# Kernel tuning notes

Measured on AMD Instinct MI355X. Metric: run time of the kernel, lower is better.

The kernel has to match this reference:

```python
import jax, jax.numpy as jnp
import numpy as np
import math

N_HEAD = 16


def setup_inputs() -> dict:
    key = jax.random.key(0)
    ks = jax.random.split(key, 9)
    B, T, D = 2, 2048, 1024
    s = 1.0 / math.sqrt(D)
    return {
        "queries": jax.random.normal(ks[0], (B, T, D), jnp.float32),
        "keys": jax.random.normal(ks[1], (B, T, D), jnp.float32),
        "key_mask": jax.random.randint(ks[2], (B, T), 0, 2, jnp.int32),
        "Wq": jax.random.normal(ks[3], (D, D), jnp.float32) * s,
        "bq": jax.random.normal(ks[4], (D,), jnp.float32) * 0.01,
        "Wk": jax.random.normal(ks[5], (D, D), jnp.float32) * s,
        "bk": jax.random.normal(ks[6], (D,), jnp.float32) * 0.01,
        "Wv": jax.random.normal(ks[7], (D, D), jnp.float32) * s,
        "bv": jax.random.normal(ks[8], (D,), jnp.float32) * 0.01,
    }


def reference(queries, keys, key_mask, Wq, bq, Wk, bk, Wv, bv):
    B, Tq, D = queries.shape
    Tk = keys.shape[1]
    H = N_HEAD
    dk = D // H
    scale = 1.0 / math.sqrt(dk)

    # torch Linear: x @ W.T + b
    Q = (queries @ Wq.T + bq).reshape(B, Tq, H, dk)
    K = (keys @ Wk.T + bk).reshape(B, Tk, H, dk)
    V = (keys @ Wv.T + bv).reshape(B, Tk, H, dk)

    # flatten batch-major over (B, H) to match torch permute+reshape -> (B*H, T, dk)
    Qf = Q.transpose(0, 2, 1, 3).reshape(B * H, Tq, dk)
    Kf = K.transpose(0, 2, 1, 3).reshape(B * H, Tk, dk)
    Vf = V.transpose(0, 2, 1, 3).reshape(B * H, Tk, dk)

    scores = jnp.einsum("nqd,nkd->nqk", Qf, Kf) * scale  # (B*H, Tq, Tk)

    # torch builds masks via .repeat(n_head,1,1): HEAD-major tiling (H copies of B).
    # flat row i of scores has batch i//H but receives mask of batch i%B —
    # reproduced faithfully here.
    km = jnp.tile(key_mask, (H, 1))  # (H*B, Tk), row j -> key_mask[j % B]
    scores = jnp.where(km[:, None, :] == 0, -1e9, scores)

    attn = jax.nn.softmax(scores, axis=-1)
    qm = jnp.tile(key_mask, (H, 1))[:, :, None].astype(attn.dtype)  # (H*B, Tk, 1), Tq==Tk
    attn = attn * qm

    # dropout: identity in eval mode
    out = jnp.einsum("nqk,nkd->nqd", attn, Vf)  # (B*H, Tq, dk)
    out = out.reshape(B, H, Tq, dk).transpose(0, 2, 1, 3).reshape(B, Tq, D)
    return out
```

## Files before the change

### kernel.cpp

```cpp
#include <hip/hip_runtime.h>
#include <hip/hip_bf16.h>

typedef __attribute__((ext_vector_type(8))) short bf16x8;
typedef __attribute__((ext_vector_type(4))) short bf16x4;
typedef __attribute__((ext_vector_type(4))) float f32x4;
typedef __attribute__((ext_vector_type(16))) float f32x16;
typedef __attribute__((ext_vector_type(4))) unsigned u32x4;

__device__ inline short f2bf(float f) {
    unsigned u = __builtin_bit_cast(unsigned, f);
    u += 0x7FFF + ((u >> 16) & 1);
    return (short)(u >> 16);
}


__global__ __launch_bounds__(256) void cvt_bf16(
    const float* __restrict__ xq, const float* __restrict__ xk,
    const float* __restrict__ Wq, const float* __restrict__ Wk,
    const float* __restrict__ Wv, const int* __restrict__ key_mask,
    short* __restrict__ ws)
{
    const int blk = blockIdx.x;
    if (blk >= 11264) {
        float* bias = (float*)(ws + 24117248u);
        const int i0 = threadIdx.x * 4;
#pragma unroll
        for (int p = 0; p < 4; ++p) {
            int idx = p * 1024 + i0;
            int4 m = *(const int4*)&key_mask[idx];
            f32x4 o = { m.x ? 0.f : -1e9f, m.y ? 0.f : -1e9f,
                        m.z ? 0.f : -1e9f, m.w ? 0.f : -1e9f };
            *(f32x4*)&bias[idx] = o;
        }
        return;
    }
    int seg, local;
    if (blk < 4096)      { seg = 0; local = blk; }
    else if (blk < 8192) { seg = 1; local = blk - 4096; }
    else                 { seg = 2 + ((blk - 8192) >> 10); local = (blk - 8192) & 1023; }
    const float* src = (seg == 0) ? xq : (seg == 1) ? xk
                     : (seg == 2) ? Wq : (seg == 3) ? Wk : Wv;
    const size_t dstoff = (seg == 0) ? 12582912u : (seg == 1) ? 16777216u
                        : 20971520u + (size_t)(seg - 2) * 1048576u;
    const size_t idx = (size_t)local * 1024 + threadIdx.x * 4;
    float4 v = *(const float4*)&src[idx];
    bf16x4 o = { f2bf(v.x), f2bf(v.y), f2bf(v.z), f2bf(v.w) };
    *(bf16x4*)&ws[dstoff + idx] = o;
}

__global__ __launch_bounds__(256) void proj_gemm(
    short* __restrict__ ws, const float* __restrict__ bq,
    const float* __restrict__ bk, const float* __restrict__ bv)
{
    const int z = blockIdx.z;
    const short* A  = ws + ((z == 0) ? 12582912u : 16777216u);
    const short* Bw = ws + 20971520u + (size_t)z * 1048576u;
    const float* bias = (z == 0) ? bq : (z == 1) ? bk : bv;
    short* out = ws + (size_t)z * 4194304u;

    const int m0 = blockIdx.x * 128;
    const int n0 = blockIdx.y * 128;
    const int tid  = threadIdx.x;
    const int lane = tid & 63;
    const int wid  = tid >> 6;
    const int wr = wid >> 1, wc = wid & 1;
    const int l15 = lane & 15, lhi = lane >> 4;

    __shared__ alignas(16) short SM[17408];

    const int srow = wid * 32 + (lane >> 2);
    const int scol = (lane & 3) * 8;
    const short* aSrc = A  + (size_t)(m0 + srow) * 1024 + scol;
    const short* bSrc = Bw + (size_t)(n0 + srow) * 1024 + scol;

#define PSTAGE(T, BUF) do {                                                    \
    _Pragma("unroll")                                                          \
    for (int i_ = 0; i_ < 2; ++i_) {                                           \
        __builtin_amdgcn_global_load_lds(                                      \
            (const __attribute__((address_space(1))) unsigned*)                \
                (aSrc + (T) * 32 + i_ * 16384),                                \
            (__attribute__((address_space(3))) unsigned*)                      \
                &SM[(BUF) * 8192 + (wid * 32 + i_ * 16) * 32], 16, 0, 0);      \
        __builtin_amdgcn_global_load_lds(                                      \
            (const __attribute__((address_space(1))) unsigned*)                \
                (bSrc + (T) * 32 + i_ * 16384),                                \
            (__attribute__((address_space(3))) unsigned*)                      \
                &SM[(BUF) * 8192 + 4096 + (wid * 32 + i_ * 16) * 32], 16, 0, 0);\
    } } while (0)

    f32x4 acc[4][4] = {};

    PSTAGE(0, 0);
    for (int t = 0; t < 32; ++t) {
        const int buf = t & 1;
        __syncthreads();
        if (t < 31) PSTAGE(t + 1, buf ^ 1);

        const short* SA = &SM[buf * 8192];
        const short* SB = SA + 4096;
        bf16x8 a[4], b[4];
#pragma unroll
        for (int i = 0; i < 4; ++i)
            a[i] = *(const bf16x8*)&SA[(wr * 64 + i * 16 + l15) * 32 + lhi * 8];
#pragma unroll
        for (int j = 0; j < 4; ++j)
            b[j] = *(const bf16x8*)&SB[(wc * 64 + j * 16 + l15) * 32 + lhi * 8];

        if (z == 2) {
#pragma unroll
            for (int i = 0; i < 4; ++i)
#pragma unroll
                for (int j = 0; j < 4; ++j)
                    acc[i][j] = __builtin_amdgcn_mfma_f32_16x16x32_bf16(
                        a[i], b[j], acc[i][j], 0, 0, 0);
        } else {
#pragma unroll
            for (int i = 0; i < 4; ++i)
#pragma unroll
                for (int j = 0; j < 4; ++j)
                    acc[i][j] = __builtin_amdgcn_mfma_f32_16x16x32_bf16(
                        b[j], a[i], acc[i][j], 0, 0, 0);
        }
    }
#undef PSTAGE

    __syncthreads();
    if (z == 2) {
#pragma unroll
        for (int i = 0; i < 4; ++i) {
            int mm = wr * 64 + i * 16 + lhi * 4;
#pragma unroll
            for (int j = 0; j < 4; ++j) {
                int nn = wc * 64 + j * 16 + l15;
                float bval = bias[n0 + nn];
                bf16x4 pk = { f2bf(acc[i][j][0] + bval), f2bf(acc[i][j][1] + bval),
                              f2bf(acc[i][j][2] + bval), f2bf(acc[i][j][3] + bval) };
                *(bf16x4*)&SM[nn * 136 + mm] = pk;
            }
        }
    } else {
#pragma unroll
        for (int i = 0; i < 4; ++i) {
            int mm = wr * 64 + i * 16 + l15;
#pragma unroll
            for (int j = 0; j < 4; ++j) {
                int nnb = wc * 64 + j * 16 + lhi * 4;
                float4 bw = *(const float4*)&bias[n0 + nnb];
                bf16x4 pk = { f2bf(acc[i][j][0] + bw.x), f2bf(acc[i][j][1] + bw.y),
                              f2bf(acc[i][j][2] + bw.z), f2bf(acc[i][j][3] + bw.w) };
                *(bf16x4*)&SM[mm * 136 + nnb] = pk;
            }
        }
    }
    __syncthreads();

    const int bb = m0 >> 11;
    const int mt = m0 & 2047;
#pragma unroll
    for (int p = 0; p < 8; ++p) {
        int id = p * 256 + tid;
        int rr = id >> 4;
        int g  = id & 15;
        bf16x8 v = *(const bf16x8*)&SM[rr * 136 + g * 8];
        if (z == 2) {
            int nn = n0 + rr, h = nn >> 6, d = nn & 63;
            *(bf16x8*)&out[(((size_t)(bb * 16 + h)) * 64 + d) * 2048 + mt + g * 8] = v;
        } else {
            int nn = n0 + g * 8, h = nn >> 6, d = nn & 63;
            *(bf16x8*)&out[(((size_t)(bb * 16 + h)) * 2048 + mt + rr) * 64 + d] = v;
        }
    }
}

__device__ inline float pair_max(float v) { return fmaxf(v, __shfl_xor(v, 32)); }
__device__ inline float pair_sum(float v) { return v + __shfl_xor(v, 32); }

__global__ __launch_bounds__(256) void attn_fwd(
    const short* __restrict__ Qb, const short* __restrict__ Kb,
    const short* __restrict__ Vtb, const int* __restrict__ key_mask,
    const float* __restrict__ biasArr, float* __restrict__ out)
{
    const int bh = blockIdx.x;
    const int qb = blockIdx.y;
    const int b  = bh >> 4;
    const int h  = bh & 15;
    const int mb = bh & 1;
    const int tid  = threadIdx.x;
    const int lane = tid & 63;
    const int wid  = tid >> 6;
    const int l31  = lane & 31;
    const int hi   = lane >> 5;

    const size_t base = (size_t)bh * 2048 * 64;
    const int q0 = qb * 128 + wid * 32;

    __shared__ alignas(16) char SMEM[34816];
#define KVS(BUF) ((short*)SMEM + (BUF) * 8192)
    float* Ld = (float*)SMEM;

    const int* km_row = key_mask + mb * 2048;
    const float* bias_row = biasArr + mb * 2048;

    bf16x8 qf[4];
#pragma unroll
    for (int ks = 0; ks < 4; ++ks)
        qf[ks] = *(const bf16x8*)&Qb[base + (size_t)(q0 + l31) * 64 + ks * 16 + hi * 8];

    const int lrow = lane >> 3;
    const int lcol = (lane & 7) ^ (lrow & 7);
    const short* srcK[2];
    const short* srcV[2];
#pragma unroll
    for (int i = 0; i < 2; ++i) {
        int r0 = wid * 16 + i * 8;
        srcK[i] = Kb  + base + (size_t)(r0 + lrow) * 64   + lcol * 8;
        srcV[i] = Vtb + base + (size_t)(r0 + lrow) * 2048 + lcol * 8;
    }

    f32x16 acc[2];
#pragma unroll
    for (int n = 0; n < 2; ++n)
#pragma unroll
        for (int r = 0; r < 16; ++r) acc[n][r] = 0.f;
    float mrun = -1e30f, lrun = 0.f;
    const float SC  = 0.18033688f;
    const float DTH = 44.3614f;

#define STAGE(T, BUF)                                                          \
    {                                                                          \
        _Pragma("unroll")                                                      \
        for (int i = 0; i < 2; ++i) {                                          \
            int r0 = wid * 16 + i * 8;                                         \
            __builtin_amdgcn_global_load_lds(                                  \
                (const __attribute__((address_space(1))) unsigned int*)        \
                    (srcK[i] + (size_t)(T) * 4096),                            \
                (__attribute__((address_space(3))) unsigned int*)              \
                    &KVS(BUF)[r0 * 64],                                        \
                16, 0, 0);                                                     \
            __builtin_amdgcn_global_load_lds(                                  \
                (const __attribute__((address_space(1))) unsigned int*)        \
                    (srcV[i] + (size_t)(T) * 64),                              \
                (__attribute__((address_space(3))) unsigned int*)              \
                    &KVS(BUF)[4096 + r0 * 64],                                 \
                16, 0, 0);                                                     \
        }                                                                      \
    }

    STAGE(0, 0);

    for (int t = 0; t < 32; ++t) {
        const int buf = t & 1;
        const int k0 = t * 64;
        __syncthreads();
        if (t < 31) STAGE(t + 1, buf ^ 1);

        const f32x4* bp = (const f32x4*)(bias_row + k0);
        f32x16 sacc[2];
#pragma unroll
        for (int s = 0; s < 2; ++s) {
#pragma unroll
            for (int g = 0; g < 4; ++g) {
                f32x4 bv = bp[s * 8 + g * 2 + hi];
#pragma unroll
                for (int c = 0; c < 4; ++c) sacc[s][g * 4 + c] = bv[c];
            }
        }
        __builtin_amdgcn_s_setprio(1);
#pragma unroll
        for (int s = 0; s < 2; ++s) {
#pragma unroll
            for (int ks = 0; ks < 4; ++ks) {
                int row = s * 32 + l31;
                int xg = ((2 * ks + hi) ^ (row & 7)) * 8;
                bf16x8 kf = *(const bf16x8*)&KVS(buf)[row * 64 + xg];
                sacc[s] = __builtin_amdgcn_mfma_f32_32x32x16_bf16(
                    kf, qf[ks], sacc[s], 0, 0, 0);
            }
        }
        __builtin_amdgcn_s_setprio(0);

        float mx = sacc[0][0];
#pragma unroll
        for (int s = 0; s < 2; ++s)
#pragma unroll
            for (int r = 0; r < 16; ++r)
                if (s + r) mx = fmaxf(mx, sacc[s][r]);
        mx = pair_max(mx);
        if (!__all(mx <= mrun + DTH)) {
            float mnew = fmaxf(mrun, mx);
            float fac  = __builtin_amdgcn_exp2f((mrun - mnew) * SC);
            lrun *= fac;
#pragma unroll
            for (int n = 0; n < 2; ++n)
#pragma unroll
                for (int r = 0; r < 16; ++r) acc[n][r] *= fac;
            mrun = mnew;
        }
        const float msc = mrun * SC;

        float p[2][16];
        float sum = 0.f;
#pragma unroll
        for (int s = 0; s < 2; ++s)
#pragma unroll
            for (int r = 0; r < 16; ++r) {
                float pe = __builtin_amdgcn_exp2f(sacc[s][r] * SC - msc);
                p[s][r] = pe;
                sum += pe;
            }
        lrun += pair_sum(sum);

        unsigned pk2[2][4][2];
#pragma unroll
        for (int s = 0; s < 2; ++s)
#pragma unroll
            for (int g = 0; g < 4; ++g)
#pragma unroll
                for (int w = 0; w < 2; ++w) {
                    unsigned d;
                    asm("v_cvt_pk_bf16_f32 %0, %1, %2"
                        : "=v"(d)
                        : "v"(p[s][g * 4 + 2 * w]), "v"(p[s][g * 4 + 2 * w + 1]));
                    pk2[s][g][w] = d;
                }

        __builtin_amdgcn_s_setprio(1);
#pragma unroll
        for (int s = 0; s < 2; ++s)
#pragma unroll
            for (int kk = 0; kk < 2; ++kk) {
                unsigned w0 = pk2[s][2 * kk][0],     w1 = pk2[s][2 * kk][1];
                unsigned w2 = pk2[s][2 * kk + 1][0], w3 = pk2[s][2 * kk + 1][1];
                asm("v_permlane32_swap_b32 %0, %1" : "+v"(w0), "+v"(w2));
                asm("v_permlane32_swap_b32 %0, %1" : "+v"(w1), "+v"(w3));
                u32x4 fv = { w0, w1, w2, w3 };
                bf16x8 pf = __builtin_bit_cast(bf16x8, fv);
                int kq = s * 2 + kk;
#pragma unroll
                for (int n = 0; n < 2; ++n) {
                    int row = n * 32 + l31;
                    int xg = ((2 * kq + hi) ^ (row & 7)) * 8;
                    bf16x8 vf = *(const bf16x8*)&KVS(buf)[4096 + row * 64 + xg];
                    acc[n] = __builtin_amdgcn_mfma_f32_32x32x16_bf16(
                        vf, pf, acc[n], 0, 0, 0);
                }
            }
        __builtin_amdgcn_s_setprio(0);
    }
#undef STAGE

    __syncthreads();

    float qn = (float)km_row[q0 + l31] / lrun;
    float* Lw = Ld + wid * 2176;
#pragma unroll
    for (int n = 0; n < 2; ++n)
#pragma unroll
        for (int r = 0; r < 16; ++r) {
            int d = n * 32 + (r & 3) + 8 * (r >> 2) + 4 * hi;
            Lw[l31 * 68 + d] = acc[n][r] * qn;
        }
    const int l15 = lane & 15, lq = lane >> 4;
#pragma unroll
    for (int rep = 0; rep < 8; ++rep) {
        int qr = rep * 4 + lq;
        f32x4 v = *(const f32x4*)&Lw[qr * 68 + l15 * 4];
        *(f32x4*)&out[((size_t)b * 2048 + q0 + qr) * 1024 + h * 64 + l15 * 4] = v;
    }
#undef KVS
}

extern "C" void kernel_launch(void* const* d_in, const int* in_sizes, int n_in,
                              void* d_out, int out_size, void* d_ws, size_t ws_size,
                              hipStream_t stream) {
    const float* queries = (const float*)d_in[0];
    const float* keys    = (const float*)d_in[1];
    const int*   key_mask= (const int*)d_in[2];
    const float* Wq = (const float*)d_in[3];
    const float* bq = (const float*)d_in[4];
    const float* Wk = (const float*)d_in[5];
    const float* bk = (const float*)d_in[6];
    const float* Wv = (const float*)d_in[7];
    const float* bv = (const float*)d_in[8];
    float* out = (float*)d_out;

    short* ws = (short*)d_ws;
    const float* biasArr = (const float*)(ws + 24117248u);

    cvt_bf16<<<11265, 256, 0, stream>>>(queries, keys, Wq, Wk, Wv, key_mask, ws);

    proj_gemm<<<dim3(32, 8, 3), 256, 0, stream>>>(ws, bq, bk, bv);

    attn_fwd<<<dim3(32, 16), 256, 0, stream>>>(
        ws, ws + 4194304, ws + 2 * 4194304, key_mask, biasArr, out);
}
```

Before: 129.2 us.

## Split attention key range across two wave groups and merge partial softmax

The attention kernel now launches 512 threads per block. Two groups of four waves each process half of the key sequence with their own double-buffered shared-memory K/V tiles, and their partial outputs, maxima and sums are merged through shared memory at the end. This is a split-K (flash-decoding-style) scheme meant to raise waves per CU and halve the serial loop length, since the grid of 512 blocks is small. The max and sum reductions are also rewritten as tree reductions to shorten dependency chains. The cost is 64KB of LDS per block, which limits occupancy, plus an extra merge step with added syncs.

Measured after the change: 122.7 us. 1.05x faster.

```diff
diff --git a/kernel.cpp b/kernel.cpp
--- a/kernel.cpp
+++ b/kernel.cpp
@@ -175,7 +175,7 @@
 __device__ inline float pair_max(float v) { return fmaxf(v, __shfl_xor(v, 32)); }
 __device__ inline float pair_sum(float v) { return v + __shfl_xor(v, 32); }
 
-__global__ __launch_bounds__(256) void attn_fwd(
+__global__ __launch_bounds__(512, 4) void attn_fwd(
     const short* __restrict__ Qb, const short* __restrict__ Kb,
     const short* __restrict__ Vtb, const int* __restrict__ key_mask,
     const float* __restrict__ biasArr, float* __restrict__ out)
@@ -188,23 +188,26 @@
     const int tid  = threadIdx.x;
     const int lane = tid & 63;
     const int wid  = tid >> 6;
+    const int qg   = wid & 3;
+    const int ks   = wid >> 2;
     const int l31  = lane & 31;
     const int hi   = lane >> 5;
 
     const size_t base = (size_t)bh * 2048 * 64;
-    const int q0 = qb * 128 + wid * 32;
-
-    __shared__ alignas(16) char SMEM[34816];
-#define KVS(BUF) ((short*)SMEM + (BUF) * 8192)
-    float* Ld = (float*)SMEM;
+    const int q0 = qb * 128 + qg * 32;
+    const int ko = ks * 1024;
+
+    __shared__ alignas(16) char SMEM[65536];
+    short* KVbase = (short*)SMEM + ks * 16384;
+#define KVS(BUF) (KVbase + (BUF) * 8192)
 
     const int* km_row = key_mask + mb * 2048;
     const float* bias_row = biasArr + mb * 2048;
 
     bf16x8 qf[4];
 #pragma unroll
-    for (int ks = 0; ks < 4; ++ks)
-        qf[ks] = *(const bf16x8*)&Qb[base + (size_t)(q0 + l31) * 64 + ks * 16 + hi * 8];
+    for (int kf = 0; kf < 4; ++kf)
+        qf[kf] = *(const bf16x8*)&Qb[base + (size_t)(q0 + l31) * 64 + kf * 16 + hi * 8];
 
     const int lrow = lane >> 3;
     const int lcol = (lane & 7) ^ (lrow & 7);
@@ -212,9 +215,9 @@
     const short* srcV[2];
 #pragma unroll
     for (int i = 0; i < 2; ++i) {
-        int r0 = wid * 16 + i * 8;
-        srcK[i] = Kb  + base + (size_t)(r0 + lrow) * 64   + lcol * 8;
-        srcV[i] = Vtb + base + (size_t)(r0 + lrow) * 2048 + lcol * 8;
+        int r0 = qg * 16 + i * 8;
+        srcK[i] = Kb  + base + (size_t)(ko + r0 + lrow) * 64 + lcol * 8;
+        srcV[i] = Vtb + base + (size_t)(r0 + lrow) * 2048 + ko + lcol * 8;
     }
 
     f32x16 acc[2];
@@ -230,7 +233,7 @@
     {                                                                          \
         _Pragma("unroll")                                                      \
         for (int i = 0; i < 2; ++i) {                                          \
-            int r0 = wid * 16 + i * 8;                                         \
+            int r0 = qg * 16 + i * 8;                                          \
             __builtin_amdgcn_global_load_lds(                                  \
                 (const __attribute__((address_space(1))) unsigned int*)        \
                     (srcK[i] + (size_t)(T) * 4096),                            \
@@ -248,11 +251,11 @@
 
     STAGE(0, 0);
 
-    for (int t = 0; t < 32; ++t) {
+    for (int t = 0; t < 16; ++t) {
         const int buf = t & 1;
-        const int k0 = t * 64;
+        const int k0 = ko + t * 64;
         __syncthreads();
-        if (t < 31) STAGE(t + 1, buf ^ 1);
+        if (t < 15) STAGE(t + 1, buf ^ 1);
 
         const f32x4* bp = (const f32x4*)(bias_row + k0);
         f32x16 sacc[2];
@@ -269,23 +272,25 @@
 #pragma unroll
         for (int s = 0; s < 2; ++s) {
 #pragma unroll
-            for (int ks = 0; ks < 4; ++ks) {
+            for (int kf = 0; kf < 4; ++kf) {
                 int row = s * 32 + l31;
-                int xg = ((2 * ks + hi) ^ (row & 7)) * 8;
-                bf16x8 kf = *(const bf16x8*)&KVS(buf)[row * 64 + xg];
+                int xg = ((2 * kf + hi) ^ (row & 7)) * 8;
+                bf16x8 kfr = *(const bf16x8*)&KVS(buf)[row * 64 + xg];
                 sacc[s] = __builtin_amdgcn_mfma_f32_32x32x16_bf16(
-                    kf, qf[ks], sacc[s], 0, 0, 0);
+                    kfr, qf[kf], sacc[s], 0, 0, 0);
             }
         }
         __builtin_amdgcn_s_setprio(0);
 
-        float mx = sacc[0][0];
-#pragma unroll
-        for (int s = 0; s < 2; ++s)
-#pragma unroll
-            for (int r = 0; r < 16; ++r)
-                if (s + r) mx = fmaxf(mx, sacc[s][r]);
-        mx = pair_max(mx);
+        float tm[16];
+#pragma unroll
+        for (int i = 0; i < 16; ++i) tm[i] = fmaxf(sacc[0][i], sacc[1][i]);
+#pragma unroll
+        for (int st = 8; st >= 1; st >>= 1)
+#pragma unroll
+            for (int i = 0; i < st; ++i) tm[i] = fmaxf(tm[i], tm[i + st]);
+        float mx = pair_max(tm[0]);
+
         if (!__all(mx <= mrun + DTH)) {
             float mnew = fmaxf(mrun, mx);
             float fac  = __builtin_amdgcn_exp2f((mrun - mnew) * SC);
@@ -299,16 +304,20 @@
         const float msc = mrun * SC;
 
         float p[2][16];
-        float sum = 0.f;
 #pragma unroll
         for (int s = 0; s < 2; ++s)
 #pragma unroll
-            for (int r = 0; r < 16; ++r) {
-                float pe = __builtin_amdgcn_exp2f(sacc[s][r] * SC - msc);
-                p[s][r] = pe;
-                sum += pe;
-            }
-        lrun += pair_sum(sum);
+            for (int r = 0; r < 16; ++r)
+                p[s][r] = __builtin_amdgcn_exp2f(sacc[s][r] * SC - msc);
+
+        float tsum[16];
+#pragma unroll
+        for (int i = 0; i < 16; ++i) tsum[i] = p[0][i] + p[1][i];
+#pragma unroll
+        for (int st = 8; st >= 1; st >>= 1)
+#pragma unroll
+            for (int i = 0; i < st; ++i) tsum[i] += tsum[i + st];
+        lrun += pair_sum(tsum[0]);
 
         unsigned pk2[2][4][2];
 #pragma unroll
@@ -348,26 +357,55 @@
         __builtin_amdgcn_s_setprio(0);
     }
 #undef STAGE
+#undef KVS
 
     __syncthreads();
-
-    float qn = (float)km_row[q0 + l31] / lrun;
-    float* Lw = Ld + wid * 2176;
-#pragma unroll
-    for (int n = 0; n < 2; ++n)
-#pragma unroll
-        for (int r = 0; r < 16; ++r) {
-            int d = n * 32 + (r & 3) + 8 * (r >> 2) + 4 * hi;
-            Lw[l31 * 68 + d] = acc[n][r] * qn;
-        }
-    const int l15 = lane & 15, lq = lane >> 4;
-#pragma unroll
-    for (int rep = 0; rep < 8; ++rep) {
-        int qr = rep * 4 + lq;
-        f32x4 v = *(const f32x4*)&Lw[qr * 68 + l15 * 4];
-        *(f32x4*)&out[((size_t)b * 2048 + q0 + qr) * 1024 + h * 64 + l15 * 4] = v;
-    }
-#undef KVS
+    float* R = (float*)SMEM + qg * 2176;
+
+    if (ks == 1) {
+#pragma unroll
+        for (int n = 0; n < 2; ++n)
+#pragma unroll
+            for (int r = 0; r < 16; ++r) {
+                int d = n * 32 + (r & 3) + 8 * (r >> 2) + 4 * hi;
+                R[d * 32 + l31] = acc[n][r];
+            }
+        if (hi == 0) { R[2048 + l31] = mrun; R[2080 + l31] = lrun; }
+    }
+    __syncthreads();
+
+    if (ks == 0) {
+        float m1 = R[2048 + l31];
+        float l1 = R[2080 + l31];
+        float o1[2][16];
+#pragma unroll
+        for (int n = 0; n < 2; ++n)
+#pragma unroll
+            for (int r = 0; r < 16; ++r) {
+                int d = n * 32 + (r & 3) + 8 * (r >> 2) + 4 * hi;
+                o1[n][r] = R[d * 32 + l31];
+            }
+        float mm = fmaxf(mrun, m1);
+        float f0 = __builtin_amdgcn_exp2f((mrun - mm) * SC);
+        float f1 = __builtin_amdgcn_exp2f((m1 - mm) * SC);
+        float lt = lrun * f0 + l1 * f1;
+        float qn = (float)km_row[q0 + l31] / lt;
+
+#pragma unroll
+        for (int n = 0; n < 2; ++n)
+#pragma unroll
+            for (int r = 0; r < 16; ++r) {
+                int d = n * 32 + (r & 3) + 8 * (r >> 2) + 4 * hi;
+                R[l31 * 68 + d] = (acc[n][r] * f0 + o1[n][r] * f1) * qn;
+            }
+        const int l15 = lane & 15, lq = lane >> 4;
+#pragma unroll
+        for (int rep = 0; rep < 8; ++rep) {
+            int qr = rep * 4 + lq;
+            f32x4 v = *(const f32x4*)&R[qr * 68 + l15 * 4];
+            *(f32x4*)&out[((size_t)b * 2048 + q0 + qr) * 1024 + h * 64 + l15 * 4] = v;
+        }
+    }
 }
 
 extern "C" void kernel_launch(void* const* d_in, const int* in_sizes, int n_in,
@@ -391,6 +429,6 @@
 
     proj_gemm<<<dim3(32, 8, 3), 256, 0, stream>>>(ws, bq, bk, bv);
 
-    attn_fwd<<<dim3(32, 16), 256, 0, stream>>>(
+    attn_fwd<<<dim3(32, 16), 512, 0, stream>>>(
         ws, ws + 4194304, ws + 2 * 4194304, key_mask, biasArr, out);
 }
```
